# Optimization experiments

Hardware: AMD Instinct MI355X
Metric: run time of the kernel (lower is better)

## Reference

```python
import jax, jax.numpy as jnp
import numpy as np

N = 100000   # num_nodes
E = 1000000  # num_edges
H = 64       # hidden_dim
M = 64       # msg_dim
C = 16       # num_classes


def setup_inputs() -> dict:
    key = jax.random.key(0)
    ks = jax.random.split(key, 16)
    s = 1.0 / np.sqrt(H)
    inp = {
        "features": jax.random.normal(ks[0], (N, H), jnp.float32),
        "src": jax.random.randint(ks[1], (E,), 0, N, dtype=jnp.int32),
        "dst": jax.random.randint(ks[2], (E,), 0, N, dtype=jnp.int32),
        "edge_types": jax.random.randint(ks[3], (E,), 0, 2, dtype=jnp.int32) == 1,
        # per-edge-type message linears (edge_matrix[0] for type==True, [1] for type==False)
        "W0": jax.random.uniform(ks[4], (M, H), jnp.float32, -s, s),
        "b0": jax.random.uniform(ks[5], (M,), jnp.float32, -s, s),
        "W1": jax.random.uniform(ks[6], (M, H), jnp.float32, -s, s),
        "b1": jax.random.uniform(ks[7], (M,), jnp.float32, -s, s),
        # GRU (single layer, single step): gates order [r, z, n] as in torch
        "W_ih": jax.random.uniform(ks[8], (3 * H, M), jnp.float32, -s, s),
        "W_hh": jax.random.uniform(ks[9], (3 * H, H), jnp.float32, -s, s),
        "b_ih": jax.random.uniform(ks[10], (3 * H,), jnp.float32, -s, s),
        "b_hh": jax.random.uniform(ks[11], (3 * H,), jnp.float32, -s, s),
        # output classifier
        "W_out": jax.random.uniform(ks[12], (C, H), jnp.float32, -s, s),
        "b_out": jax.random.uniform(ks[13], (C,), jnp.float32, -s, s),
    }
    return inp


def reference(features, src, dst, edge_types,
              W0, b0, W1, b1, W_ih, W_hh, b_ih, b_hh, W_out, b_out):
    # gather source-node features per edge: [E, H]
    x = features[src]
    # tiny per-edge-type linear; select by edge type
    m0 = x @ W0.T + b0            # type True  -> edge_matrix[0]
    m1 = x @ W1.T + b1            # type False -> edge_matrix[1]
    msg = jnp.where(edge_types[:, None], m0, m1)  # [E, M]
    # scatter-add messages into node buffer (zero-initialized accumulator)
    agg = jax.ops.segment_sum(msg, dst, num_segments=N)  # [N, M]
    # single GRU step: input=agg, hidden=features
    gi = agg @ W_ih.T + b_ih       # [N, 3H]
    gh = features @ W_hh.T + b_hh  # [N, 3H]
    i_r, i_z, i_n = jnp.split(gi, 3, axis=-1)
    h_r, h_z, h_n = jnp.split(gh, 3, axis=-1)
    r = jax.nn.sigmoid(i_r + h_r)
    z = jax.nn.sigmoid(i_z + h_z)
    n = jnp.tanh(i_n + r * h_n)
    h = (1.0 - z) * n + z * features  # [N, H]
    # output classifier
    return h @ W_out.T + b_out        # [N, C]
```

## Files before the change

kernel.cpp:

```cpp
#include <hip/hip_runtime.h>


typedef __bf16 bf16x8 __attribute__((ext_vector_type(8)));
typedef float  f32x4  __attribute__((ext_vector_type(4)));
typedef int    i32x4  __attribute__((ext_vector_type(4)));

#define MFMA16 __builtin_amdgcn_mfma_f32_16x16x32_bf16
#define NN   100000
#define EE   1000000
#define BB   782
#define NPB  128
#define ECAP 1600
#define DCAP 48
#define CSTRD 49
#define NB   245
#define NWL  24576

__device__ __forceinline__ float sigmoidf_(float x) {
    return 1.0f / (1.0f + __expf(-x));
}

__device__ __forceinline__ bf16x8 ldw(const __bf16* w, int e) {
    int bo = e * 2;
    bo ^= ((bo >> 7) & 7) << 4;
    return *(const bf16x8*)((const char*)w + bo);
}

__global__ __launch_bounds__(256) void k_init(const unsigned char* __restrict__ et,
                                              const float* __restrict__ feat,
                                              const int* __restrict__ dst,
                                              const float* __restrict__ w0,
                                              const float* __restrict__ w1,
                                              const float* __restrict__ wih,
                                              const float* __restrict__ whh,
                                              const float* __restrict__ wout,
                                              __bf16* __restrict__ featb,
                                              __bf16* __restrict__ wb,
                                              int* __restrict__ hist,
                                              int* __restrict__ flag) {
    int b = blockIdx.x, tid = threadIdx.x;
    if (b == 0) {
        __shared__ int sdet[4];
        const i32x4* p = (const i32x4*)et + tid * 16;
        unsigned acc = 0;
#pragma unroll
        for (int j = 0; j < 16; j++) {
            i32x4 w = p[j];
            acc |= (unsigned)(w[0] | w[1] | w[2] | w[3]) & 0xffffff00u;
        }
        unsigned long long m = __ballot(acc != 0);
        if ((tid & 63) == 0) sdet[tid >> 6] = (m != 0ULL);
        __syncthreads();
        if (tid == 0) *flag = sdet[0] | sdet[1] | sdet[2] | sdet[3];
        return;
    }
    if (b < 133) {
        int i = (b - 1) * 256 + tid;
        float v;
        if      (i < 4096)  v = w0[i];
        else if (i < 8192)  v = w1[i - 4096];
        else if (i < 20480) v = wih[i - 8192];
        else if (i < 32768) v = whh[i - 20480];
        else                v = wout[i - 32768];
        wb[i] = (__bf16)v;
        return;
    }
    if (b >= 6383) {
        __shared__ int cnt[BB];
        int hb = b - 6383;
        for (int i = tid; i < BB; i += 256) cnt[i] = 0;
        __syncthreads();
        long e0 = (long)hb * 4096 + tid * 16;
#pragma unroll
        for (int g = 0; g < 2; g++) {
            long e = e0 + g * 8;
            if (e < EE) {
                i32x4 d0 = *(const i32x4*)(dst + e);
                i32x4 d1 = *(const i32x4*)(dst + e + 4);
#pragma unroll
                for (int j = 0; j < 4; j++) atomicAdd(&cnt[d0[j] >> 7], 1);
#pragma unroll
                for (int j = 0; j < 4; j++) atomicAdd(&cnt[d1[j] >> 7], 1);
            }
        }
        __syncthreads();
        for (int i = tid; i < BB; i += 256) hist[hb * BB + i] = cnt[i];
        return;
    }
    long i = ((long)(b - 133) * 256 + tid) * 4;
    if (i >= (long)NN * 64) return;
    f32x4 v = *(const f32x4*)(feat + i);
    union { __bf16 e[4]; unsigned long long u; } o;
#pragma unroll
    for (int j = 0; j < 4; j++) o.e[j] = (__bf16)v[j];
    *(unsigned long long*)(featb + i) = o.u;
}

__global__ __launch_bounds__(256) void k_s2(const int* __restrict__ hist,
                                            int* __restrict__ blockBase,
                                            int* __restrict__ bucketCnt) {
    int b = blockIdx.x * 4 + (threadIdx.x >> 6);
    int lane = threadIdx.x & 63;
    if (b >= BB) return;
    int carry = 0;
    for (int c = 0; c < 4; c++) {
        int blk = c * 64 + lane;
        int v = (blk < NB) ? hist[blk * BB + b] : 0;
        int x = v;
#pragma unroll
        for (int off = 1; off < 64; off <<= 1) {
            int y = __shfl_up(x, off, 64);
            if (lane >= off) x += y;
        }
        if (blk < NB) blockBase[blk * BB + b] = x - v + carry;
        carry += __shfl(x, 63, 64);
    }
    if (lane == 0) bucketCnt[b] = carry;
}

__global__ __launch_bounds__(512) void k_s3(const int* __restrict__ src,
                                            const int* __restrict__ dst,
                                            const unsigned char* __restrict__ etype,
                                            const int* __restrict__ flag,
                                            const int* __restrict__ blockBase,
                                            int* __restrict__ region) {
    __shared__ int cur[BB];
    int blk = blockIdx.x, tid = threadIdx.x;
    for (int i = tid; i < BB; i += 512) cur[i] = blockBase[blk * BB + i];
    __syncthreads();
    long e0 = (long)blk * 4096 + tid * 8;
    if (e0 >= EE) return;
    i32x4 s0 = *(const i32x4*)(src + e0);
    i32x4 s1 = *(const i32x4*)(src + e0 + 4);
    i32x4 d0 = *(const i32x4*)(dst + e0);
    i32x4 d1 = *(const i32x4*)(dst + e0 + 4);
    int t[8];
    if (*flag) {
        unsigned long long w = *(const unsigned long long*)(etype + e0);
#pragma unroll
        for (int j = 0; j < 8; j++) t[j] = (int)((w >> (8 * j)) & 0xff);
    } else {
        i32x4 w0 = *(const i32x4*)((const int*)etype + e0);
        i32x4 w1 = *(const i32x4*)((const int*)etype + e0 + 4);
#pragma unroll
        for (int j = 0; j < 4; j++) { t[j] = w0[j]; t[4 + j] = w1[j]; }
    }
    int dd[8] = {d0[0], d0[1], d0[2], d0[3], d1[0], d1[1], d1[2], d1[3]};
    int ss[8] = {s0[0], s0[1], s0[2], s0[3], s1[0], s1[1], s1[2], s1[3]};
#pragma unroll
    for (int j = 0; j < 8; j++) {
        int b  = dd[j] >> 7;
        int nl = dd[j] & 127;
        int r  = atomicAdd(&cur[b], 1);
        if (r < ECAP)
            region[b * ECAP + r] = (nl << 18) | ((t[j] ? 1 : 0) << 17) | ss[j];
    }
}

__global__ __launch_bounds__(512, 4) void k_gm(const __bf16* __restrict__ featb,
                                               const int* __restrict__ region,
                                               const int* __restrict__ bucketCnt,
                                               const float* __restrict__ feat,
                                               const __bf16* __restrict__ wb,
                                               const float* __restrict__ b0,
                                               const float* __restrict__ b1,
                                               const float* __restrict__ bih,
                                               const float* __restrict__ bhh,
                                               const float* __restrict__ bout,
                                               float* __restrict__ out) {
    __shared__ __align__(16) __bf16 wlds[NWL];
    __shared__ __align__(16) int csr[NPB * CSTRD];
    __shared__ int ncnt[NPB];
    int b = blockIdx.x, tid = threadIdx.x, lane = tid & 63, wave = tid >> 6;
    int L = lane & 15, q = lane >> 4;
    int n0 = b * NPB + wave * 16;

    bf16x8 Aft[2];
    if (n0 < NN) {
        const __bf16* fr = featb + (long)(n0 + L) * 64;
        Aft[0] = *(const bf16x8*)(fr + q * 8);
        Aft[1] = *(const bf16x8*)(fr + 32 + q * 8);
    }

    int cntE = min(bucketCnt[b], ECAP);
    if (tid < NPB) ncnt[tid] = 0;
    __syncthreads();
    const int* reg = region + b * ECAP;
    for (int i = tid; i < cntE; i += 512) {
        int rec = reg[i];
        int nl = rec >> 18;
        int r = atomicAdd(&ncnt[nl], 1);
        if (r < DCAP) csr[nl * CSTRD + r] = rec & 0x3ffff;
    }
    const __bf16* wsrc = wb + 8192;
    for (int k = tid * 8; k < NWL; k += 512 * 8) {
        bf16x8 v = *(const bf16x8*)(wsrc + k);
        int bo = k * 2;
        int so = bo ^ (((bo >> 7) & 7) << 4);
        *(bf16x8*)((char*)wlds + so) = v;
    }
    __syncthreads();

    int nl = wave * 16 + L;
    int cnt = (n0 < NN) ? min(ncnt[nl], DCAP) : 0;
    const int* eb = &csr[nl * CSTRD];

    float sA[16], s1[16];
#pragma unroll
    for (int j = 0; j < 16; j++) { sA[j] = 0.f; s1[j] = 0.f; }
    int c1 = 0;
    int i = 0;
    for (; i + 2 <= cnt; i += 2) {
        int ea = eb[i], ebn = eb[i + 1];
        const __bf16* rowa = featb + (long)(ea & 0x1ffff) * 64;
        const __bf16* rowb = featb + (long)(ebn & 0x1ffff) * 64;
        bf16x8 a0 = *(const bf16x8*)(rowa + q * 8);
        bf16x8 a1 = *(const bf16x8*)(rowa + 32 + q * 8);
        bf16x8 b0v = *(const bf16x8*)(rowb + q * 8);
        bf16x8 b1v = *(const bf16x8*)(rowb + 32 + q * 8);
        int ta = (ea >> 17) & 1, tb = (ebn >> 17) & 1;
        c1 += ta + tb;
        float fa = (float)ta, fb = (float)tb;
#pragma unroll
        for (int j = 0; j < 8; j++) {
            float va = (float)a0[j], wa = (float)a1[j];
            float vb = (float)b0v[j], wb2 = (float)b1v[j];
            sA[j]     += va + vb;
            sA[8 + j] += wa + wb2;
            s1[j]     += fa * va + fb * vb;
            s1[8 + j] += fa * wa + fb * wb2;
        }
    }
    if (i < cnt) {
        int ea = eb[i];
        const __bf16* rowa = featb + (long)(ea & 0x1ffff) * 64;
        bf16x8 a0 = *(const bf16x8*)(rowa + q * 8);
        bf16x8 a1 = *(const bf16x8*)(rowa + 32 + q * 8);
        int ta = (ea >> 17) & 1;
        c1 += ta;
        float fa = (float)ta;
#pragma unroll
        for (int j = 0; j < 8; j++) {
            float va = (float)a0[j], wa = (float)a1[j];
            sA[j] += va;          sA[8 + j] += wa;
            s1[j] += fa * va;     s1[8 + j] += fa * wa;
        }
    }
    if (n0 >= NN) return;

    bf16x8 AS1[2], AS0[2];
    {
        union { bf16x8 v; __bf16 e[8]; } u;
#pragma unroll
        for (int ch = 0; ch < 2; ch++) {
#pragma unroll
            for (int j = 0; j < 8; j++) u.e[j] = (__bf16)s1[ch * 8 + j];
            AS1[ch] = u.v;
#pragma unroll
            for (int j = 0; j < 8; j++) u.e[j] = (__bf16)(sA[ch * 8 + j] - s1[ch * 8 + j]);
            AS0[ch] = u.v;
        }
    }
    int ccp = cnt | (c1 << 16);
    float fc1[4], fc0[4];
#pragma unroll
    for (int r = 0; r < 4; r++) {
        int v = __shfl(ccp, q * 4 + r, 64);
        int c1v = v >> 16;
        fc1[r] = (float)c1v; fc0[r] = (float)((v & 0xffff) - c1v);
    }

    __bf16* sH = (__bf16*)((char*)csr + wave * (16 * CSTRD * 4));
    const __bf16* w0b = wb, * w1b = wb + 4096, * woutb = wb + 32768;
    f32x4 zz = {0.f, 0.f, 0.f, 0.f};

#pragma unroll
    for (int nb = 0; nb < 4; nb++) {
        f32x4 acc = zz;
#pragma unroll
        for (int ch = 0; ch < 2; ch++) {
            int off = (nb * 16 + L) * 64 + ch * 32 + q * 8;
            acc = MFMA16(AS1[ch], *(const bf16x8*)(w0b + off), acc, 0, 0, 0);
            acc = MFMA16(AS0[ch], *(const bf16x8*)(w1b + off), acc, 0, 0, 0);
        }
        float bs0 = b0[nb * 16 + L], bs1 = b1[nb * 16 + L];
#pragma unroll
        for (int r = 0; r < 4; r++)
            sH[(q * 4 + r) * 80 + nb * 16 + L] =
                (__bf16)(acc[r] + fc1[r] * bs0 + fc0[r] * bs1);
    }

    bf16x8 Aag[2];
#pragma unroll
    for (int ch = 0; ch < 2; ch++)
        Aag[ch] = *(const bf16x8*)&sH[L * 80 + ch * 32 + q * 8];

#pragma unroll
    for (int nb = 0; nb < 4; nb++) {
        int row = nb * 16 + L;
        float fvb[4];
#pragma unroll
        for (int r = 0; r < 4; r++)
            fvb[r] = feat[(long)(n0 + q * 4 + r) * 64 + nb * 16 + L];
        f32x4 aR = zz, aZ = zz, aIN = zz, aHN = zz;
#pragma unroll
        for (int ch = 0; ch < 2; ch++) {
            int ko = ch * 32 + q * 8;
            aR  = MFMA16(Aag[ch], ldw(wlds, row * 64 + ko), aR, 0, 0, 0);
            aR  = MFMA16(Aft[ch], ldw(wlds, 12288 + row * 64 + ko), aR, 0, 0, 0);
            aZ  = MFMA16(Aag[ch], ldw(wlds, (64 + row) * 64 + ko), aZ, 0, 0, 0);
            aZ  = MFMA16(Aft[ch], ldw(wlds, 12288 + (64 + row) * 64 + ko), aZ, 0, 0, 0);
            aIN = MFMA16(Aag[ch], ldw(wlds, (128 + row) * 64 + ko), aIN, 0, 0, 0);
            aHN = MFMA16(Aft[ch], ldw(wlds, 12288 + (128 + row) * 64 + ko), aHN, 0, 0, 0);
        }
        int h = row;
        float br  = bih[h] + bhh[h];
        float bz  = bih[64 + h] + bhh[64 + h];
        float bin = bih[128 + h];
        float bhn = bhh[128 + h];
#pragma unroll
        for (int r = 0; r < 4; r++) {
            float rv = sigmoidf_(aR[r] + br);
            float zv = sigmoidf_(aZ[r] + bz);
            float nv = tanhf(aIN[r] + bin + rv * (aHN[r] + bhn));
            float fv = fvb[r];
            sH[(q * 4 + r) * 80 + h] = (__bf16)((1.0f - zv) * nv + zv * fv);
        }
    }

    bf16x8 Ah0 = *(const bf16x8*)&sH[L * 80 + q * 8];
    bf16x8 Ah1 = *(const bf16x8*)&sH[L * 80 + 32 + q * 8];
    bf16x8 Bo0 = *(const bf16x8*)(woutb + L * 64 + q * 8);
    bf16x8 Bo1 = *(const bf16x8*)(woutb + L * 64 + 32 + q * 8);
    f32x4 o = zz;
    o = MFMA16(Ah0, Bo0, o, 0, 0, 0);
    o = MFMA16(Ah1, Bo1, o, 0, 0, 0);
    float bo = bout[L];
#pragma unroll
    for (int r = 0; r < 4; r++)
        out[(long)(n0 + q * 4 + r) * 16 + L] = o[r] + bo;
}

extern "C" void kernel_launch(void* const* d_in, const int* in_sizes, int n_in,
                              void* d_out, int out_size, void* d_ws, size_t ws_size,
                              hipStream_t stream) {
    const float* features = (const float*)d_in[0];
    const int*   src      = (const int*)d_in[1];
    const int*   dst      = (const int*)d_in[2];
    const unsigned char* etype = (const unsigned char*)d_in[3];
    const float* W0   = (const float*)d_in[4];
    const float* b0   = (const float*)d_in[5];
    const float* W1   = (const float*)d_in[6];
    const float* b1   = (const float*)d_in[7];
    const float* Wih  = (const float*)d_in[8];
    const float* Whh  = (const float*)d_in[9];
    const float* bih  = (const float*)d_in[10];
    const float* bhh  = (const float*)d_in[11];
    const float* Wout = (const float*)d_in[12];
    const float* bout = (const float*)d_in[13];
    float* out = (float*)d_out;

    char* ws = (char*)d_ws;
    size_t off = 0;
    __bf16* featb     = (__bf16*)(ws + off); off += (size_t)NN * 64 * 2;
    int*    region    = (int*)(ws + off);    off += (size_t)BB * ECAP * 4;
    int*    hist      = (int*)(ws + off);    off += (size_t)NB * BB * 4;
    int*    blockBase = (int*)(ws + off);    off += (size_t)NB * BB * 4;
    int*    bucketCnt = (int*)(ws + off);    off += (size_t)BB * 4;
    __bf16* wb        = (__bf16*)(ws + off); off += 33792 * 2;
    int*    flag      = (int*)(ws + off);

    k_init<<<6628, 256, 0, stream>>>(etype, features, dst, W0, W1, Wih, Whh,
                                     Wout, featb, wb, hist, flag);
    k_s2<<<(BB + 3) / 4, 256, 0, stream>>>(hist, blockBase, bucketCnt);
    k_s3<<<NB, 512, 0, stream>>>(src, dst, etype, flag, blockBase, region);
    k_gm<<<BB, 512, 0, stream>>>(featb, region, bucketCnt, features, wb,
                                 b0, b1, bih, bhh, bout, out);
}
```

Baseline: 173.2 us.

## Replace per-node CSR gather with LDS atomic scatter-add of edge features

Drops the per-block CSR build and the per-node gather loop. Each thread now takes one edge record, loads its whole 64-element source row and atomically adds it into one of two per-type fp32 accumulators in LDS, plus counts. After that, shared memory is reused for the weights and the hidden-state staging. This removes the degree cap (DCAP) and the load imbalance across nodes, but issues 64 LDS float atomics per edge and adds extra barriers and a zeroing pass.

```diff
diff --git a/kernel.cpp b/kernel.cpp
--- a/kernel.cpp
+++ b/kernel.cpp
@@ -11,10 +11,9 @@
 #define BB   782
 #define NPB  128
 #define ECAP 1600
-#define DCAP 48
-#define CSTRD 49
 #define NB   245
 #define NWL  24576
+#define ASTR 65
 
 __device__ __forceinline__ float sigmoidf_(float x) {
     return 1.0f / (1.0f + __expf(-x));
@@ -168,109 +167,86 @@
                                                const float* __restrict__ bhh,
                                                const float* __restrict__ bout,
                                                float* __restrict__ out) {
-    __shared__ __align__(16) __bf16 wlds[NWL];
-    __shared__ __align__(16) int csr[NPB * CSTRD];
-    __shared__ int ncnt[NPB];
+    __shared__ __align__(16) char smem[69632];
+    __shared__ int ncntA[NPB];
+    __shared__ int c1nA[NPB];
     int b = blockIdx.x, tid = threadIdx.x, lane = tid & 63, wave = tid >> 6;
     int L = lane & 15, q = lane >> 4;
     int n0 = b * NPB + wave * 16;
 
+    float* acc1 = (float*)smem;
+    float* acc0 = (float*)(smem + NPB * ASTR * 4);
+
+    f32x4 z4 = {0.f, 0.f, 0.f, 0.f};
+    for (int i = tid; i < 4160; i += 512) ((f32x4*)smem)[i] = z4;
+    if (tid < NPB) { ncntA[tid] = 0; c1nA[tid] = 0; }
+    __syncthreads();
+
+    int cntE = min(bucketCnt[b], ECAP);
+    const int* reg = region + b * ECAP;
+    for (int e = tid; e < cntE; e += 512) {
+        int rec = reg[e];
+        int nl = rec >> 18;
+        int ty = (rec >> 17) & 1;
+        const bf16x8* row = (const bf16x8*)(featb + (long)(rec & 0x1ffff) * 64);
+        bf16x8 fr8[8];
+#pragma unroll
+        for (int f = 0; f < 8; f++) fr8[f] = row[f];
+        float* pa = (ty ? acc1 : acc0) + nl * ASTR;
+#pragma unroll
+        for (int f = 0; f < 8; f++)
+#pragma unroll
+            for (int j = 0; j < 8; j++)
+                atomicAdd(&pa[f * 8 + j], (float)fr8[f][j]);
+        atomicAdd(&ncntA[nl], 1);
+        if (ty) atomicAdd(&c1nA[nl], 1);
+    }
+    __syncthreads();
+
+    bf16x8 AS1[2], AS0[2];
+    float fc1[4], fc0[4];
+    int nl = wave * 16 + L;
+    if (n0 < NN) {
+        union { bf16x8 v; __bf16 e[8]; } u;
+#pragma unroll
+        for (int ch = 0; ch < 2; ch++) {
+            const float* p1 = acc1 + nl * ASTR + ch * 32 + q * 8;
+            const float* p0 = acc0 + nl * ASTR + ch * 32 + q * 8;
+#pragma unroll
+            for (int j = 0; j < 8; j++) u.e[j] = (__bf16)p1[j];
+            AS1[ch] = u.v;
+#pragma unroll
+            for (int j = 0; j < 8; j++) u.e[j] = (__bf16)p0[j];
+            AS0[ch] = u.v;
+        }
+#pragma unroll
+        for (int r = 0; r < 4; r++) {
+            int node = wave * 16 + q * 4 + r;
+            int c1v = c1nA[node];
+            fc1[r] = (float)c1v;
+            fc0[r] = (float)(ncntA[node] - c1v);
+        }
+    }
+    __syncthreads();
+
+    const __bf16* wsrc = wb + 8192;
+    __bf16* wlds = (__bf16*)smem;
+    for (int k = tid * 8; k < NWL; k += 512 * 8) {
+        bf16x8 v = *(const bf16x8*)(wsrc + k);
+        int bo = k * 2;
+        int so = bo ^ (((bo >> 7) & 7) << 4);
+        *(bf16x8*)((char*)smem + so) = v;
+    }
     bf16x8 Aft[2];
     if (n0 < NN) {
         const __bf16* fr = featb + (long)(n0 + L) * 64;
         Aft[0] = *(const bf16x8*)(fr + q * 8);
         Aft[1] = *(const bf16x8*)(fr + 32 + q * 8);
     }
-
-    int cntE = min(bucketCnt[b], ECAP);
-    if (tid < NPB) ncnt[tid] = 0;
-    __syncthreads();
-    const int* reg = region + b * ECAP;
-    for (int i = tid; i < cntE; i += 512) {
-        int rec = reg[i];
-        int nl = rec >> 18;
-        int r = atomicAdd(&ncnt[nl], 1);
-        if (r < DCAP) csr[nl * CSTRD + r] = rec & 0x3ffff;
-    }
-    const __bf16* wsrc = wb + 8192;
-    for (int k = tid * 8; k < NWL; k += 512 * 8) {
-        bf16x8 v = *(const bf16x8*)(wsrc + k);
-        int bo = k * 2;
-        int so = bo ^ (((bo >> 7) & 7) << 4);
-        *(bf16x8*)((char*)wlds + so) = v;
-    }
-    __syncthreads();
-
-    int nl = wave * 16 + L;
-    int cnt = (n0 < NN) ? min(ncnt[nl], DCAP) : 0;
-    const int* eb = &csr[nl * CSTRD];
-
-    float sA[16], s1[16];
-#pragma unroll
-    for (int j = 0; j < 16; j++) { sA[j] = 0.f; s1[j] = 0.f; }
-    int c1 = 0;
-    int i = 0;
-    for (; i + 2 <= cnt; i += 2) {
-        int ea = eb[i], ebn = eb[i + 1];
-        const __bf16* rowa = featb + (long)(ea & 0x1ffff) * 64;
-        const __bf16* rowb = featb + (long)(ebn & 0x1ffff) * 64;
-        bf16x8 a0 = *(const bf16x8*)(rowa + q * 8);
-        bf16x8 a1 = *(const bf16x8*)(rowa + 32 + q * 8);
-        bf16x8 b0v = *(const bf16x8*)(rowb + q * 8);
-        bf16x8 b1v = *(const bf16x8*)(rowb + 32 + q * 8);
-        int ta = (ea >> 17) & 1, tb = (ebn >> 17) & 1;
-        c1 += ta + tb;
-        float fa = (float)ta, fb = (float)tb;
-#pragma unroll
-        for (int j = 0; j < 8; j++) {
-            float va = (float)a0[j], wa = (float)a1[j];
-            float vb = (float)b0v[j], wb2 = (float)b1v[j];
-            sA[j]     += va + vb;
-            sA[8 + j] += wa + wb2;
-            s1[j]     += fa * va + fb * vb;
-            s1[8 + j] += fa * wa + fb * wb2;
-        }
-    }
-    if (i < cnt) {
-        int ea = eb[i];
-        const __bf16* rowa = featb + (long)(ea & 0x1ffff) * 64;
-        bf16x8 a0 = *(const bf16x8*)(rowa + q * 8);
-        bf16x8 a1 = *(const bf16x8*)(rowa + 32 + q * 8);
-        int ta = (ea >> 17) & 1;
-        c1 += ta;
-        float fa = (float)ta;
-#pragma unroll
-        for (int j = 0; j < 8; j++) {
-            float va = (float)a0[j], wa = (float)a1[j];
-            sA[j] += va;          sA[8 + j] += wa;
-            s1[j] += fa * va;     s1[8 + j] += fa * wa;
-        }
-    }
+    __syncthreads();
     if (n0 >= NN) return;
 
-    bf16x8 AS1[2], AS0[2];
-    {
-        union { bf16x8 v; __bf16 e[8]; } u;
-#pragma unroll
-        for (int ch = 0; ch < 2; ch++) {
-#pragma unroll
-            for (int j = 0; j < 8; j++) u.e[j] = (__bf16)s1[ch * 8 + j];
-            AS1[ch] = u.v;
-#pragma unroll
-            for (int j = 0; j < 8; j++) u.e[j] = (__bf16)(sA[ch * 8 + j] - s1[ch * 8 + j]);
-            AS0[ch] = u.v;
-        }
-    }
-    int ccp = cnt | (c1 << 16);
-    float fc1[4], fc0[4];
-#pragma unroll
-    for (int r = 0; r < 4; r++) {
-        int v = __shfl(ccp, q * 4 + r, 64);
-        int c1v = v >> 16;
-        fc1[r] = (float)c1v; fc0[r] = (float)((v & 0xffff) - c1v);
-    }
-
-    __bf16* sH = (__bf16*)((char*)csr + wave * (16 * CSTRD * 4));
+    __bf16* sH = (__bf16*)(smem + 49152 + wave * 2560);
     const __bf16* w0b = wb, * w1b = wb + 4096, * woutb = wb + 32768;
     f32x4 zz = {0.f, 0.f, 0.f, 0.f};
 
```

New measurement: 548.9 us. 217% more time.
